# Optimization experiments

Hardware: AMD Instinct MI355X
Metric: run time of the kernel (lower is better)

## Reference

```python
import math
import jax, jax.numpy as jnp
import numpy as np

NUM_HEADS = 16
D_MODEL = 1024
WINDOW = 512


def alibi_slopes(num_heads):
    # 1 / ((2**8)**((i+1)/num_heads))  for i in range(num_heads)
    x = (2.0 ** 8) ** (1.0 / num_heads)
    return jnp.asarray([1.0 / x ** (i + 1) for i in range(num_heads)], dtype=jnp.float32)


def setup_inputs() -> dict:
    key = jax.random.key(0)
    k1, k2 = jax.random.split(key)
    x = jax.random.normal(k1, (1, 4096, D_MODEL), dtype=jnp.float32)
    # scale weight like a trained init so softmax isn't saturated
    w_kqv = jax.random.normal(k2, (D_MODEL, 3 * D_MODEL), dtype=jnp.float32) * 0.02
    return {"x": x, "w_kqv": w_kqv}


def reference(x, w_kqv):
    B, S, D = x.shape
    H = NUM_HEADS
    hd = D // H
    scale = math.sqrt(D)  # module scales by sqrt(d_model), not sqrt(head_dim)

    kqv = x @ w_kqv                       # [B, S, 3D]
    k, q, v = jnp.split(kqv, 3, axis=-1)  # chunk order: key, query, value
    k = k.reshape(B, S, H, hd).transpose(0, 2, 1, 3)  # [B, H, S, hd]
    q = q.reshape(B, S, H, hd).transpose(0, 2, 1, 3)
    v = v.reshape(B, S, H, hd).transpose(0, 2, 1, 3)

    # ALiBi bias: m_h * (j - i)
    pos = jnp.arange(S)
    rel = pos[None, :] - pos[:, None]                  # [S, S] = x - y
    bias = alibi_slopes(H)[:, None, None] * rel.astype(jnp.float32)  # [H, S, S]

    score = jnp.einsum("bhqd,bhkd->bhqk", q, k) / scale + bias[None]

    # causal sliding-window mask: allow 0 <= i - j <= WINDOW
    dist = pos[:, None] - pos[None, :]                 # i - j
    mask = (dist >= 0) & (dist <= WINDOW)              # [S, S]
    score = jnp.where(mask[None, None], score, -jnp.inf)

    attn = jax.nn.softmax(score, axis=-1)
    out = jnp.einsum("bhqk,bhkd->bhqd", attn, v)       # [B, H, S, hd]
    out = out.transpose(0, 2, 1, 3).reshape(B, S, D)
    return out
```

## Files before the change

kernel.cpp:

```cpp
#include <hip/hip_runtime.h>
#include <hip/hip_bf16.h>

#define SEQ   4096
#define DM    1024
#define NH    16
#define HD    64
#define N3    3072
#define WIN   512

#define LOG2E 1.4426950408889634f

typedef __attribute__((ext_vector_type(8))) short short8;
typedef __attribute__((ext_vector_type(4))) short short4v;
typedef __attribute__((ext_vector_type(4))) float float4v;

__device__ __forceinline__ float bf16_bits_to_float(unsigned short u) {
  return __uint_as_float(((unsigned int)u) << 16);
}

typedef __attribute__((address_space(3))) void lds_void_t;
typedef __attribute__((address_space(1))) const void gbl_void_t;
__device__ __forceinline__ void async_copy16(void* lds_dst, const void* g_src) {
  __builtin_amdgcn_global_load_lds((gbl_void_t*)g_src, (lds_void_t*)lds_dst,
                                   16, 0, 0);
}

template <int NT>
__device__ __forceinline__ int detect_fp32(const unsigned short* __restrict__ probe,
                                           float* red) {
  const int t = threadIdx.x;
  float mx = 0.0f;
#pragma unroll
  for (int p = 0; p < 8; ++p) {
    float v = bf16_bits_to_float(probe[(t * 8 + p) * 2]);
    if (v != v) v = 1e38f;
    mx = fmaxf(mx, fabsf(v));
  }
  red[t] = mx;
  __syncthreads();
  for (int s = NT / 2; s > 0; s >>= 1) {
    if (t < s) red[t] = fmaxf(red[t], red[t + s]);
    __syncthreads();
  }
  const int fl = red[0] > 100.0f ? 1 : 0;
  __syncthreads();
  return fl;
}

__device__ __forceinline__ int detect_fp32_wave(
    const unsigned short* __restrict__ probe) {
  const int lane = threadIdx.x & 63;
  float mx = 0.0f;
#pragma unroll
  for (int p = 0; p < 8; ++p) {
    float v = bf16_bits_to_float(probe[(lane * 8 + p) * 2]);
    if (v != v) v = 1e38f;
    mx = fmaxf(mx, fabsf(v));
  }
  return __any(mx > 100.0f) ? 1 : 0;
}

__global__ __launch_bounds__(256) void prep(
    const void* __restrict__ x, const void* __restrict__ w,
    __hip_bfloat16* __restrict__ xb, __hip_bfloat16* __restrict__ wt) {
  __shared__ __hip_bfloat16 tile[64][66];
  __shared__ float red[256];
  const int t = threadIdx.x;
  if (blockIdx.x < 2048) {
    const int fl = detect_fp32<256>((const unsigned short*)x, red);
    const int i0 = (blockIdx.x * 256 + t) * 8;
    if (fl) {
      const float* xf = (const float*)x + i0;
      float4 f0 = *(const float4*)(xf);
      float4 f1 = *(const float4*)(xf + 4);
      __hip_bfloat16 tmp[8];
      tmp[0] = __float2bfloat16(f0.x); tmp[1] = __float2bfloat16(f0.y);
      tmp[2] = __float2bfloat16(f0.z); tmp[3] = __float2bfloat16(f0.w);
      tmp[4] = __float2bfloat16(f1.x); tmp[5] = __float2bfloat16(f1.y);
      tmp[6] = __float2bfloat16(f1.z); tmp[7] = __float2bfloat16(f1.w);
      *(uint4*)&xb[i0] = *(const uint4*)tmp;
    } else {
      *(uint4*)&xb[i0] = *(const uint4*)((const __hip_bfloat16*)x + i0);
    }
  } else {
    const int bid = blockIdx.x - 2048;
    const int fl = detect_fp32<256>((const unsigned short*)w, red);
    const int n0 = (bid % 48) * 64;
    const int k0 = (bid / 48) * 64;
    const int tx = t & 63, ty0 = t >> 6;
    if (fl) {
      const float* wf = (const float*)w;
#pragma unroll
      for (int p = 0; p < 16; ++p) {
        int row = ty0 + p * 4;
        tile[row][tx] = __float2bfloat16(wf[(k0 + row) * N3 + n0 + tx]);
      }
    } else {
      const __hip_bfloat16* wb = (const __hip_bfloat16*)w;
#pragma unroll
      for (int p = 0; p < 16; ++p) {
        int row = ty0 + p * 4;
        tile[row][tx] = wb[(k0 + row) * N3 + n0 + tx];
      }
    }
    __syncthreads();
#pragma unroll
    for (int r = 0; r < 2; ++r) {
      int oe = r * 2048 + t * 8;
      int nr = oe >> 6, kc = oe & 63;
      __hip_bfloat16 v[8];
#pragma unroll
      for (int e = 0; e < 8; ++e) v[e] = tile[kc + e][nr];
      *(uint4*)&wt[(n0 + nr) * DM + k0 + kc] = *(const uint4*)v;
    }
  }
}

__global__ __launch_bounds__(256) void gemm_kqv(
    const __hip_bfloat16* __restrict__ A,
    const __hip_bfloat16* __restrict__ BT,
    __hip_bfloat16* __restrict__ C) {
  __shared__ __align__(16) __hip_bfloat16 As[2][128 * 32];
  __shared__ __align__(16) __hip_bfloat16 Bs[2][128 * 32];
  const int m0 = blockIdx.y * 128;
  const int n0 = blockIdx.x * 128;
  const int t = threadIdx.x;
  const int wave = t >> 6, lane = t & 63;
  const int wm = wave >> 1, wn = wave & 1;
  const int l15 = lane & 15, quad = lane >> 4;

  const int srow0 = wave * 16 + (lane >> 2);
  const int scol  = (lane & 3) * 8;
  const int sbyte = wave * 1024 + lane * 16;

  float4v acc[4][4] = {};

  for (int k0 = 0; k0 < DM; k0 += 64) {
    __syncthreads();
#pragma unroll
    for (int half = 0; half < 2; ++half) {
      const int kk = k0 + half * 32;
#pragma unroll
      for (int r = 0; r < 2; ++r) {
        const int row = srow0 + r * 64;
        async_copy16((char*)As[half] + r * 4096 + sbyte,
                     &A[(m0 + row) * DM + kk + scol]);
        async_copy16((char*)Bs[half] + r * 4096 + sbyte,
                     &BT[(n0 + row) * DM + kk + scol]);
      }
    }
    __syncthreads();

#pragma unroll
    for (int half = 0; half < 2; ++half) {
      short8 a[4], b[4];
#pragma unroll
      for (int mi = 0; mi < 4; ++mi)
        a[mi] = *(const short8*)(&As[half][(wm * 64 + mi * 16 + l15) * 32 + quad * 8]);
#pragma unroll
      for (int ni = 0; ni < 4; ++ni)
        b[ni] = *(const short8*)(&Bs[half][(wn * 64 + ni * 16 + l15) * 32 + quad * 8]);
#pragma unroll
      for (int mi = 0; mi < 4; ++mi)
#pragma unroll
        for (int ni = 0; ni < 4; ++ni)
          acc[mi][ni] = __builtin_amdgcn_mfma_f32_16x16x32_bf16(
              a[mi], b[ni], acc[mi][ni], 0, 0, 0);
    }
  }

#pragma unroll
  for (int mi = 0; mi < 4; ++mi)
#pragma unroll
    for (int ni = 0; ni < 4; ++ni)
#pragma unroll
      for (int r = 0; r < 4; ++r) {
        int row = m0 + wm * 64 + mi * 16 + quad * 4 + r;
        int col = n0 + wn * 64 + ni * 16 + l15;
        C[row * N3 + col] = __float2bfloat16(acc[mi][ni][r]);
      }
}

__global__ __launch_bounds__(256, 4) void attn(
    const __hip_bfloat16* __restrict__ kqv,
    const unsigned short* __restrict__ xprobe,
    void* __restrict__ out) {
  __shared__ __align__(16) __hip_bfloat16 Ks[64 * 72];
  __shared__ __align__(16) __hip_bfloat16 Vt[80 * 72];
  __shared__ __align__(16) __hip_bfloat16 Ps[64 * 72];

  const int fl = detect_fp32_wave(xprobe);
  const int h  = blockIdx.y;
  const int bx = blockIdx.x;
  const int i0 = 64 * ((bx & 7) * 8 + (bx >> 3));
  const int t    = threadIdx.x;
  const int wave = t >> 6, lane = t & 63;
  const int l15 = lane & 15, quad = lane >> 4;
  const float slope2  = exp2f(-0.5f * (float)(h + 1)) * LOG2E;
  const float nslope2 = -slope2;
  const float qscale  = LOG2E / 32.0f;

  for (int idx = t; idx < 16 * 64; idx += 256) {
    int rr = idx >> 6, cc = idx & 63;
    ((unsigned short*)Vt)[(64 + rr) * 72 + cc] = (rr == 0) ? 0x3F80 : 0;
  }

  short8 aq[2];
#pragma unroll
  for (int ks2 = 0; ks2 < 2; ++ks2)
    aq[ks2] = *(const short8*)&kqv[(i0 + wave * 16 + l15) * N3 + DM + h * HD +
                                   ks2 * 32 + quad * 8];

  float4v o[5] = {};

  const int jlo  = max(0, i0 - WIN);
  const int nblk = (i0 + 64 - jlo) >> 6;

  const int krow0 = t >> 3, krow1 = (t >> 3) + 32, kd0 = (t & 7) * 8;
  const int rbase = t >> 3;
  const int vd0   = (t & 7) * 8;
  const int kA    = (rbase & 15) + ((rbase >> 4) << 5);
  const int vsig2 = (((rbase & 15) << 2) + ((rbase >> 4) << 1)) * 2;
  const int vswz  = (t & 7) << 4;
  uint4 kregA, kregB, vregA, vregB;
  kregA = *(const uint4*)&kqv[(jlo + krow0) * N3 + h * HD + kd0];
  kregB = *(const uint4*)&kqv[(jlo + krow1) * N3 + h * HD + kd0];
  vregA = *(const uint4*)&kqv[(jlo + kA) * N3 + 2 * DM + h * HD + vd0];
  vregB = *(const uint4*)&kqv[(jlo + kA + 16) * N3 + 2 * DM + h * HD + vd0];

  for (int b = 0; b < nblk; ++b) {
    const int j0 = jlo + b * 64;
    __syncthreads();
    *(uint4*)&Ks[krow0 * 72 + kd0] = kregA;
    *(uint4*)&Ks[krow1 * 72 + kd0] = kregB;
    {
      const unsigned short* pa = (const unsigned short*)&vregA;
      const unsigned short* pb = (const unsigned short*)&vregB;
      char* vbase = (char*)Vt;
#pragma unroll
      for (int e = 0; e < 8; ++e) {
        unsigned int pack = (unsigned int)pa[e] | ((unsigned int)pb[e] << 16);
        *(unsigned int*)(vbase + (vd0 + e) * 144 + (vsig2 ^ vswz)) = pack;
      }
    }
    __syncthreads();

    if (b + 1 < nblk) {
      const int jn = j0 + 64;
      kregA = *(const uint4*)&kqv[(jn + krow0) * N3 + h * HD + kd0];
      kregB = *(const uint4*)&kqv[(jn + krow1) * N3 + h * HD + kd0];
      vregA = *(const uint4*)&kqv[(jn + kA) * N3 + 2 * DM + h * HD + vd0];
      vregB = *(const uint4*)&kqv[(jn + kA + 16) * N3 + 2 * DM + h * HD + vd0];
    }

    float4v sacc[4] = {};
#pragma unroll
    for (int ks2 = 0; ks2 < 2; ++ks2)
#pragma unroll
      for (int nt = 0; nt < 4; ++nt) {
        short8 bk = *(const short8*)&Ks[(nt * 16 + l15) * 72 + ks2 * 32 + quad * 8];
        sacc[nt] = __builtin_amdgcn_mfma_f32_16x16x32_bf16(aq[ks2], bk, sacc[nt], 0, 0, 0);
      }

    const int dbase = (i0 + wave * 16 + quad * 4) - (j0 + l15);
    const float s16 = nslope2 * -16.0f;
    const int psbase = (wave * 16 + quad * 4) * 72 + l15 * 4;
#pragma unroll
    for (int r = 0; r < 4; ++r) {
      float bias = nslope2 * (float)(dbase + r);
      int rel = dbase + r;
      short4v pk;
#pragma unroll
      for (int nt = 0; nt < 4; ++nt) {
        float x = fmaf(sacc[nt][r], qscale, bias);
        x = ((unsigned)rel <= (unsigned)WIN) ? x : -200.0f;
        __hip_bfloat16 hb = __float2bfloat16(exp2f(x));
        pk[nt] = *reinterpret_cast<const short*>(&hb);
        bias += s16;
        rel -= 16;
      }
      *(short4v*)&Ps[psbase + r * 72] = pk;
    }

#pragma unroll
    for (int ks = 0; ks < 64; ks += 32) {
      short8 ap = *(const short8*)&Ps[(wave * 16 + l15) * 72 + ks + quad * 8];
#pragma unroll
      for (int dt = 0; dt < 5; ++dt) {
        const int vrow = dt * 16 + l15;
        const short8 bv = *(const short8*)((const char*)Vt + vrow * 144 +
            ((ks * 2 + (quad << 4)) ^ (((vrow >> 3) & 7) << 4)));
        o[dt] = __builtin_amdgcn_mfma_f32_16x16x32_bf16(ap, bv, o[dt], 0, 0, 0);
      }
    }
  }

#pragma unroll
  for (int r = 0; r < 4; ++r) {
    const float l = __shfl(o[4][r], quad * 16, 64);
    const float inv_l = 1.0f / l;
    const int row = i0 + wave * 16 + quad * 4 + r;
#pragma unroll
    for (int dt = 0; dt < 4; ++dt) {
      const int idx = row * DM + h * HD + dt * 16 + l15;
      const float v = o[dt][r] * inv_l;
      if (fl) ((float*)out)[idx] = v;
      else    ((__hip_bfloat16*)out)[idx] = __float2bfloat16(v);
    }
  }
}

extern "C" void kernel_launch(void* const* d_in, const int* in_sizes, int n_in,
                              void* d_out, int out_size, void* d_ws, size_t ws_size,
                              hipStream_t stream) {
  char* ws = (char*)d_ws;
  __hip_bfloat16* wt  = (__hip_bfloat16*)(ws + 4096);
  __hip_bfloat16* kqv = (__hip_bfloat16*)(ws + 4096 + 6291456);
  __hip_bfloat16* xb  = (__hip_bfloat16*)d_out;

  hipLaunchKernelGGL(prep, dim3(2048 + 768), dim3(256), 0, stream,
                     d_in[0], d_in[1], xb, wt);
  hipLaunchKernelGGL(gemm_kqv, dim3(24, 32), dim3(256), 0, stream, xb, wt, kqv);
  hipLaunchKernelGGL(attn, dim3(64, 16), dim3(256), 0, stream,
                     kqv, (const unsigned short*)d_in[0], d_out);
}
```

Baseline: 148.5 us.

## Rewrite KQV GEMM with 256x256 tiles and triple-buffered async pipeline

The QKV projection GEMM moves from 128x128 tiles with 256 threads and a double sync per k-step to 256x256 tiles with 512 threads. It uses a three-stage async global-to-LDS ring, interleaves the next-stage loads with MFMA work, raises wave priority around MFMA bursts, and swizzles block indices for L2 locality. The goal is to hide global load latency and raise data reuse per tile. In exchange it uses more LDS and registers per block, and the 192-block grid may underfill the 256 CUs.

```diff
diff --git a/kernel.cpp b/kernel.cpp
--- a/kernel.cpp
+++ b/kernel.cpp
@@ -116,66 +116,103 @@
   }
 }
 
-__global__ __launch_bounds__(256) void gemm_kqv(
+__global__ __launch_bounds__(512, 2) void gemm_kqv(
     const __hip_bfloat16* __restrict__ A,
     const __hip_bfloat16* __restrict__ BT,
     __hip_bfloat16* __restrict__ C) {
-  __shared__ __align__(16) __hip_bfloat16 As[2][128 * 32];
-  __shared__ __align__(16) __hip_bfloat16 Bs[2][128 * 32];
-  const int m0 = blockIdx.y * 128;
-  const int n0 = blockIdx.x * 128;
+  __shared__ __align__(16) __hip_bfloat16 As[3][256 * 32];
+  __shared__ __align__(16) __hip_bfloat16 Bs[3][256 * 32];
+
+  const int flat = blockIdx.y * 12 + blockIdx.x;
+  const int swz  = (flat & 7) * 24 + (flat >> 3);
+  const int m0 = (swz / 12) * 256;
+  const int n0 = (swz % 12) * 256;
+
   const int t = threadIdx.x;
   const int wave = t >> 6, lane = t & 63;
-  const int wm = wave >> 1, wn = wave & 1;
+  const int wm = wave >> 2, wn = wave & 3;
   const int l15 = lane & 15, quad = lane >> 4;
 
-  const int srow0 = wave * 16 + (lane >> 2);
-  const int scol  = (lane & 3) * 8;
-  const int sbyte = wave * 1024 + lane * 16;
-
-  float4v acc[4][4] = {};
-
-  for (int k0 = 0; k0 < DM; k0 += 64) {
-    __syncthreads();
-#pragma unroll
-    for (int half = 0; half < 2; ++half) {
-      const int kk = k0 + half * 32;
-#pragma unroll
-      for (int r = 0; r < 2; ++r) {
-        const int row = srow0 + r * 64;
-        async_copy16((char*)As[half] + r * 4096 + sbyte,
-                     &A[(m0 + row) * DM + kk + scol]);
-        async_copy16((char*)Bs[half] + r * 4096 + sbyte,
-                     &BT[(n0 + row) * DM + kk + scol]);
-      }
-    }
-    __syncthreads();
-
-#pragma unroll
-    for (int half = 0; half < 2; ++half) {
-      short8 a[4], b[4];
-#pragma unroll
-      for (int mi = 0; mi < 4; ++mi)
-        a[mi] = *(const short8*)(&As[half][(wm * 64 + mi * 16 + l15) * 32 + quad * 8]);
+  const int srow = t >> 2;
+  const int scol = (t & 3) * 8;
+  const __hip_bfloat16* gA0 = &A [(m0 +       srow) * DM + scol];
+  const __hip_bfloat16* gA1 = &A [(m0 + 128 + srow) * DM + scol];
+  const __hip_bfloat16* gB0 = &BT[(n0 +       srow) * DM + scol];
+  const __hip_bfloat16* gB1 = &BT[(n0 + 128 + srow) * DM + scol];
+  const int ldst = t * 16;
+
+#define STAGE_A(buf, kt) do { \
+    const int ko_ = (kt) * 32; \
+    async_copy16((char*)As[buf] + ldst,        gA0 + ko_); \
+    async_copy16((char*)As[buf] + 8192 + ldst, gA1 + ko_); } while (0)
+#define STAGE_B(buf, kt) do { \
+    const int ko_ = (kt) * 32; \
+    async_copy16((char*)Bs[buf] + ldst,        gB0 + ko_); \
+    async_copy16((char*)Bs[buf] + 8192 + ldst, gB1 + ko_); } while (0)
+
+  const int arow = wm * 128 + l15;
+  const int brow = wn * 64 + l15;
+  const int kbyte = quad * 16;
+
+  float4v acc[8][4] = {};
+
+  STAGE_A(0, 0); STAGE_B(0, 0);
+  STAGE_A(1, 1); STAGE_B(1, 1);
+  asm volatile("s_waitcnt vmcnt(4)" ::: "memory");
+  __builtin_amdgcn_s_barrier();
+
+  for (int kt = 0; kt < 32; ++kt) {
+    const int cur = kt % 3;
+    const int nb  = (kt + 2) % 3;
+    const char* Ac = (const char*)As[cur];
+    const char* Bc = (const char*)Bs[cur];
+    short8 a[4], b[4];
+
+    if (kt < 30) STAGE_A(nb, kt + 2);
+#pragma unroll
+    for (int mi = 0; mi < 4; ++mi)
+      a[mi] = *(const short8*)(Ac + (arow + mi * 16) * 64 + kbyte);
+#pragma unroll
+    for (int ni = 0; ni < 4; ++ni)
+      b[ni] = *(const short8*)(Bc + (brow + ni * 16) * 64 + kbyte);
+    __builtin_amdgcn_s_barrier();
+    __builtin_amdgcn_s_setprio(1);
+#pragma unroll
+    for (int mi = 0; mi < 4; ++mi)
 #pragma unroll
       for (int ni = 0; ni < 4; ++ni)
-        b[ni] = *(const short8*)(&Bs[half][(wn * 64 + ni * 16 + l15) * 32 + quad * 8]);
-#pragma unroll
-      for (int mi = 0; mi < 4; ++mi)
-#pragma unroll
-        for (int ni = 0; ni < 4; ++ni)
-          acc[mi][ni] = __builtin_amdgcn_mfma_f32_16x16x32_bf16(
-              a[mi], b[ni], acc[mi][ni], 0, 0, 0);
-    }
-  }
-
-#pragma unroll
-  for (int mi = 0; mi < 4; ++mi)
+        acc[mi][ni] = __builtin_amdgcn_mfma_f32_16x16x32_bf16(
+            a[mi], b[ni], acc[mi][ni], 0, 0, 0);
+    __builtin_amdgcn_s_setprio(0);
+
+    if (kt < 30) STAGE_B(nb, kt + 2);
+#pragma unroll
+    for (int mi = 0; mi < 4; ++mi)
+      a[mi] = *(const short8*)(Ac + (arow + 64 + mi * 16) * 64 + kbyte);
+    __builtin_amdgcn_s_barrier();
+    __builtin_amdgcn_s_setprio(1);
+#pragma unroll
+    for (int mi = 0; mi < 4; ++mi)
+#pragma unroll
+      for (int ni = 0; ni < 4; ++ni)
+        acc[4 + mi][ni] = __builtin_amdgcn_mfma_f32_16x16x32_bf16(
+            a[mi], b[ni], acc[4 + mi][ni], 0, 0, 0);
+    __builtin_amdgcn_s_setprio(0);
+
+    if (kt <= 28) asm volatile("s_waitcnt vmcnt(4)" ::: "memory");
+    else          asm volatile("s_waitcnt vmcnt(0)" ::: "memory");
+    __builtin_amdgcn_s_barrier();
+  }
+#undef STAGE_A
+#undef STAGE_B
+
+#pragma unroll
+  for (int mi = 0; mi < 8; ++mi)
 #pragma unroll
     for (int ni = 0; ni < 4; ++ni)
 #pragma unroll
       for (int r = 0; r < 4; ++r) {
-        int row = m0 + wm * 64 + mi * 16 + quad * 4 + r;
+        int row = m0 + wm * 128 + mi * 16 + quad * 4 + r;
         int col = n0 + wn * 64 + ni * 16 + l15;
         C[row * N3 + col] = __float2bfloat16(acc[mi][ni][r]);
       }
@@ -320,7 +357,7 @@
 
   hipLaunchKernelGGL(prep, dim3(2048 + 768), dim3(256), 0, stream,
                      d_in[0], d_in[1], xb, wt);
-  hipLaunchKernelGGL(gemm_kqv, dim3(24, 32), dim3(256), 0, stream, xb, wt, kqv);
+  hipLaunchKernelGGL(gemm_kqv, dim3(12, 16), dim3(512), 0, stream, xb, wt, kqv);
   hipLaunchKernelGGL(attn, dim3(64, 16), dim3(256), 0, stream,
                      kqv, (const unsigned short*)d_in[0], d_out);
 }
```

Result: slower. 154.1 us (+3.7%).

## Restructure KQV GEMM with 128x192 tiles, double-buffered async loads, swizzled LDS

Applied to the files above, without the earlier changes.

Rewrites the projection GEMM to use 512-thread blocks with 128x192 tiles. Global-to-LDS copies are double-buffered so the next K tile loads while MFMAs run on the current one, with explicit vmcnt waits and barriers. LDS layouts are XOR-swizzled to avoid bank conflicts, the block order is swizzled for L2 locality, and s_setprio raises priority around the MFMA sections. The cost is more LDS and registers per block and a more fragile hand-written synchronisation scheme.

```diff
diff --git a/kernel.cpp b/kernel.cpp
--- a/kernel.cpp
+++ b/kernel.cpp
@@ -116,67 +116,102 @@
   }
 }
 
-__global__ __launch_bounds__(256) void gemm_kqv(
+__global__ __launch_bounds__(512, 2) void gemm_kqv(
     const __hip_bfloat16* __restrict__ A,
     const __hip_bfloat16* __restrict__ BT,
     __hip_bfloat16* __restrict__ C) {
-  __shared__ __align__(16) __hip_bfloat16 As[2][128 * 32];
-  __shared__ __align__(16) __hip_bfloat16 Bs[2][128 * 32];
-  const int m0 = blockIdx.y * 128;
-  const int n0 = blockIdx.x * 128;
+  __shared__ __align__(16) __hip_bfloat16 As[2][2][128 * 32];
+  __shared__ __align__(16) __hip_bfloat16 Bs[2][192 * 64];
+
+  const int flat = blockIdx.y * 16 + blockIdx.x;
+  const int swz  = (flat & 7) * 64 + (flat >> 3);
+  const int m0 = (swz >> 4) * 128;
+  const int n0 = (swz & 15) * 192;
+
   const int t = threadIdx.x;
   const int wave = t >> 6, lane = t & 63;
-  const int wm = wave >> 1, wn = wave & 1;
+  const int wm = wave >> 2, wn = wave & 3;
   const int l15 = lane & 15, quad = lane >> 4;
 
-  const int srow0 = wave * 16 + (lane >> 2);
-  const int scol  = (lane & 3) * 8;
-  const int sbyte = wave * 1024 + lane * 16;
-
-  float4v acc[4][4] = {};
-
-  for (int k0 = 0; k0 < DM; k0 += 64) {
-    __syncthreads();
-#pragma unroll
-    for (int half = 0; half < 2; ++half) {
-      const int kk = k0 + half * 32;
-#pragma unroll
-      for (int r = 0; r < 2; ++r) {
-        const int row = srow0 + r * 64;
-        async_copy16((char*)As[half] + r * 4096 + sbyte,
-                     &A[(m0 + row) * DM + kk + scol]);
-        async_copy16((char*)Bs[half] + r * 4096 + sbyte,
-                     &BT[(n0 + row) * DM + kk + scol]);
-      }
-    }
-    __syncthreads();
-
-#pragma unroll
-    for (int half = 0; half < 2; ++half) {
-      short8 a[4], b[4];
+  const int arow = t >> 2;
+  const int acol = ((t & 3) ^ (arow & 3)) * 8;
+  const long aoff = (long)(m0 + arow) * DM + acol;
+  const int brow = t >> 3;
+  const int bcol = ((t & 7) ^ (brow & 7)) * 8;
+  const long boff0 = (long)(n0 +       brow) * DM + bcol;
+  const long boff1 = (long)(n0 +  64 + brow) * DM + bcol;
+  const long boff2 = (long)(n0 + 128 + brow) * DM + bcol;
+  const int ldst = t * 16;
+
+#define STAGE_B(buf, kt) do { \
+    const int ko_ = (kt) * 64; \
+    async_copy16((char*)Bs[buf]         + ldst, &BT[boff0 + ko_]); \
+    async_copy16((char*)Bs[buf] +  8192 + ldst, &BT[boff1 + ko_]); \
+    async_copy16((char*)Bs[buf] + 16384 + ldst, &BT[boff2 + ko_]); } while (0)
+#define STAGE_A(buf, kt) do { \
+    const int ko_ = (kt) * 64; \
+    async_copy16((char*)As[buf][0] + ldst, &A[aoff + ko_]); \
+    async_copy16((char*)As[buf][1] + ldst, &A[aoff + ko_ + 32]); } while (0)
+
+  float4v acc[4][3] = {};
+
+  STAGE_B(0, 0); STAGE_A(0, 0);
+  asm volatile("s_waitcnt vmcnt(0)" ::: "memory");
+  __builtin_amdgcn_s_barrier();
+
+  for (int kt = 0; kt < 16; ++kt) {
+    const int P = kt & 1, N = P ^ 1;
+    short8 a[4], b[3];
+
+#pragma unroll
+    for (int h = 0; h < 2; ++h) {
+      const char* Ap = (const char*)As[P][h];
+      const char* Bp = (const char*)Bs[P];
+#pragma unroll
+      for (int mi = 0; mi < 4; ++mi) {
+        const int row = wm * 64 + mi * 16 + l15;
+        a[mi] = *(const short8*)(Ap + row * 64 + ((quad ^ (row & 3)) << 4));
+      }
+#pragma unroll
+      for (int ni = 0; ni < 3; ++ni) {
+        const int row = wn * 48 + ni * 16 + l15;
+        b[ni] = *(const short8*)(Bp + row * 128 +
+                                 ((((h << 2) + quad) ^ (row & 7)) << 4));
+      }
+      if (h == 0) {
+        if (kt < 15) {
+          STAGE_B(N, kt + 1);
+          asm volatile("s_waitcnt vmcnt(3)" ::: "memory");
+        } else {
+          asm volatile("s_waitcnt vmcnt(0)" ::: "memory");
+        }
+      } else {
+        if (kt < 15) STAGE_A(N, kt + 1);
+        asm volatile("s_waitcnt vmcnt(1)" ::: "memory");
+      }
+      __builtin_amdgcn_s_barrier();
+      __builtin_amdgcn_s_setprio(1);
 #pragma unroll
       for (int mi = 0; mi < 4; ++mi)
-        a[mi] = *(const short8*)(&As[half][(wm * 64 + mi * 16 + l15) * 32 + quad * 8]);
-#pragma unroll
-      for (int ni = 0; ni < 4; ++ni)
-        b[ni] = *(const short8*)(&Bs[half][(wn * 64 + ni * 16 + l15) * 32 + quad * 8]);
-#pragma unroll
-      for (int mi = 0; mi < 4; ++mi)
-#pragma unroll
-        for (int ni = 0; ni < 4; ++ni)
+#pragma unroll
+        for (int ni = 0; ni < 3; ++ni)
           acc[mi][ni] = __builtin_amdgcn_mfma_f32_16x16x32_bf16(
               a[mi], b[ni], acc[mi][ni], 0, 0, 0);
-    }
-  }
+      __builtin_amdgcn_s_setprio(0);
+      __builtin_amdgcn_s_barrier();
+    }
+  }
+#undef STAGE_A
+#undef STAGE_B
 
 #pragma unroll
   for (int mi = 0; mi < 4; ++mi)
 #pragma unroll
-    for (int ni = 0; ni < 4; ++ni)
+    for (int ni = 0; ni < 3; ++ni)
 #pragma unroll
       for (int r = 0; r < 4; ++r) {
         int row = m0 + wm * 64 + mi * 16 + quad * 4 + r;
-        int col = n0 + wn * 64 + ni * 16 + l15;
+        int col = n0 + wn * 48 + ni * 16 + l15;
         C[row * N3 + col] = __float2bfloat16(acc[mi][ni][r]);
       }
 }
@@ -320,7 +355,7 @@
 
   hipLaunchKernelGGL(prep, dim3(2048 + 768), dim3(256), 0, stream,
                      d_in[0], d_in[1], xb, wt);
-  hipLaunchKernelGGL(gemm_kqv, dim3(24, 32), dim3(256), 0, stream, xb, wt, kqv);
+  hipLaunchKernelGGL(gemm_kqv, dim3(16, 32), dim3(512), 0, stream, xb, wt, kqv);
   hipLaunchKernelGGL(attn, dim3(64, 16), dim3(256), 0, stream,
                      kqv, (const unsigned short*)d_in[0], d_out);
 }
```

New measurement: 141.7 us. 1.05x faster.
